# Kernel optimization log

Measured on AMD Instinct MI355X. Metric: run time of the kernel, lower is better.

The kernel has to match this reference:

```python
import jax, jax.numpy as jnp
import numpy as np

V, E, H, B, T = 50257, 1024, 1024, 64, 512  # vocab, embed, hidden, batch, steps
PADDING_TOKEN = 0


def setup_inputs() -> dict:
    key = jax.random.key(0)
    ks = jax.random.split(key, 6)
    s = 0.02
    emb = jax.random.normal(ks[0], (V, E), jnp.float32) * s
    emb = emb.at[PADDING_TOKEN].set(0.0)  # padding_idx row is zero
    W_ih = jax.random.normal(ks[1], (4 * H, E), jnp.float32) * s   # torch LSTMCell weight_ih
    W_hh = jax.random.normal(ks[2], (4 * H, H), jnp.float32) * s   # torch LSTMCell weight_hh
    W_cls = jax.random.normal(ks[3], (V, H), jnp.float32) * s      # classifier weight [out,in]
    b_cls = jnp.zeros((V,), jnp.float32)                            # classifier bias
    batch_reviews = jax.random.randint(ks[4], (B, T), 0, V)
    return dict(batch_reviews=batch_reviews, emb=emb, W_ih=W_ih, W_hh=W_hh,
                W_cls=W_cls, b_cls=b_cls)


def _lstm_scan(x_tbe, W_ih, W_hh):
    # torch.nn.LSTMCell math (bias=False); gate order: i, f, g, o
    Bn = x_tbe.shape[1]
    Hn = W_hh.shape[1]

    def cell(carry, x_be):
        h, c = carry
        gates = x_be @ W_ih.T + h @ W_hh.T              # [B, 4H]
        i, f, g, o = jnp.split(gates, 4, axis=-1)
        c2 = jax.nn.sigmoid(f) * c + jax.nn.sigmoid(i) * jnp.tanh(g)
        h2 = jax.nn.sigmoid(o) * jnp.tanh(c2)
        return (h2, c2), None

    init = (jnp.zeros((Bn, Hn), x_tbe.dtype), jnp.zeros((Bn, Hn), x_tbe.dtype))
    (h, c), _ = jax.lax.scan(cell, init, x_tbe)
    return h, c


def reference(batch_reviews, emb, W_ih, W_hh, W_cls, b_cls):
    x = emb[batch_reviews]               # [B, T, E] embedding lookup
    x_tbe = jnp.transpose(x, (1, 0, 2))  # [T, B, E] for time-major scan
    h, c = _lstm_scan(x_tbe, W_ih, W_hh) # final (h, c) state only
    logits = h @ W_cls.T + b_cls         # [B, V]
    return logits, h, c
```

## Files before the change

kernel.cpp:

```cpp
#include <hip/hip_runtime.h>

#define Bn 64
#define Tn 512
#define En 1024
#define Hn 1024
#define Vn 50257
#define CHUNK 64
#define NCHUNK (Tn / CHUNK)
#define AGENT __HIP_MEMORY_SCOPE_AGENT

typedef __attribute__((ext_vector_type(8))) short short8;
typedef __attribute__((ext_vector_type(4))) float f32x4;
typedef __attribute__((ext_vector_type(4))) unsigned int u32x4;

__device__ __forceinline__ unsigned short f2bf(float f) {
    union { float f; unsigned u; } x; x.f = f;
    unsigned r = x.u + 0x7FFFu + ((x.u >> 16) & 1u);
    return (unsigned short)(r >> 16);
}
__device__ __forceinline__ float bf2f(unsigned short u) {
    union { unsigned u; float f; } x; x.u = ((unsigned)u) << 16; return x.f;
}
__device__ __forceinline__ float sigm(float x) { return 1.0f / (1.0f + __expf(-x)); }
__device__ __forceinline__ float tanh_fast(float x) {
    float e = __expf(2.0f * x);
    return (e - 1.0f) / (e + 1.0f);
}

#define LDH(dst, base, IMM)                                                  \
    asm volatile("global_load_dwordx4 %0, %1, off offset:" #IMM " sc0 sc1"   \
                 : "=v"(dst) : "v"(base) : "memory")
#define VMW(N) do { asm volatile("s_waitcnt vmcnt(" #N ")" ::: "memory");    \
                    __builtin_amdgcn_sched_barrier(0); } while (0)
#define ISSUE_GRP(buf, O0, O1, O2, O3)                                       \
    do {                                                                     \
        LDH((buf)[0], ap0, O0); LDH((buf)[1], ap0, O1);                      \
        LDH((buf)[2], ap0, O2); LDH((buf)[3], ap0, O3);                      \
        LDH((buf)[4], ap1, O0); LDH((buf)[5], ap1, O1);                      \
        LDH((buf)[6], ap1, O2); LDH((buf)[7], ap1, O3);                      \
    } while (0)
#define MFMA_GRP(buf, jb)                                                    \
    do {                                                                     \
        _Pragma("unroll")                                                    \
        for (int jj = 0; jj < 4; ++jj) {                                     \
            union { u32x4 u; short8 s; } f0, f1;                             \
            f0.u = (buf)[jj]; f1.u = (buf)[4 + jj];                          \
            acc[0][0] = __builtin_amdgcn_mfma_f32_16x16x32_bf16(f0.s, breg[0][(jb) + jj], acc[0][0], 0, 0, 0); \
            acc[0][1] = __builtin_amdgcn_mfma_f32_16x16x32_bf16(f0.s, breg[1][(jb) + jj], acc[0][1], 0, 0, 0); \
            acc[1][0] = __builtin_amdgcn_mfma_f32_16x16x32_bf16(f1.s, breg[0][(jb) + jj], acc[1][0], 0, 0, 0); \
            acc[1][1] = __builtin_amdgcn_mfma_f32_16x16x32_bf16(f1.s, breg[1][(jb) + jj], acc[1][1], 0, 0, 0); \
        }                                                                    \
    } while (0)

__global__ __launch_bounds__(256)
void cvt_f32_bf16(const float* __restrict__ src, unsigned short* __restrict__ dst, int n4) {
    int i = blockIdx.x * 256 + threadIdx.x;
    if (i < n4) {
        float4 v = reinterpret_cast<const float4*>(src)[i];
        ushort4 o;
        o.x = f2bf(v.x); o.y = f2bf(v.y); o.z = f2bf(v.z); o.w = f2bf(v.w);
        reinterpret_cast<ushort4*>(dst)[i] = o;
    }
}

__global__ __launch_bounds__(256)
void gather_x(const int* __restrict__ tokens, const float* __restrict__ emb,
              unsigned short* __restrict__ X, int t0) {
    const int r = blockIdx.x;
    const int trel = r >> 6, b = r & 63;
    const int tok = tokens[b * Tn + t0 + trel];
    const float* src = emb + (size_t)tok * En;
    const int k = threadIdx.x * 4;
    float4 v = *reinterpret_cast<const float4*>(src + k);
    ushort4 o;
    o.x = f2bf(v.x); o.y = f2bf(v.y); o.z = f2bf(v.z); o.w = f2bf(v.w);
    *reinterpret_cast<ushort4*>(X + (size_t)r * En + k) = o;
}

__device__ __forceinline__ void gemm_tile(
    const unsigned short* __restrict__ X, const unsigned short* __restrict__ Wih,
    unsigned short* __restrict__ G, int bx, int by,
    unsigned short (*As)[72], unsigned short (*Bs)[72], int tid)
{
    const int w = tid >> 6, l = tid & 63;
    const int wr = w >> 1, wc = w & 1;
    const int koff = (l >> 4) * 8;

    f32x4 acc[4][4];
#pragma unroll
    for (int i = 0; i < 4; ++i)
#pragma unroll
        for (int j = 0; j < 4; ++j) acc[i][j] = (f32x4){0.f, 0.f, 0.f, 0.f};

    for (int kk = 0; kk < En / 64; ++kk) {
        __syncthreads();
#pragma unroll
        for (int j = 0; j < 4; ++j) {
            const int u = tid * 4 + j;
            const int row = u >> 3, ku = (u & 7) * 8;
            *reinterpret_cast<short8*>(&As[row][ku]) =
                *reinterpret_cast<const short8*>(X + (size_t)(by * 128 + row) * En + kk * 64 + ku);
            *reinterpret_cast<short8*>(&Bs[row][ku]) =
                *reinterpret_cast<const short8*>(Wih + (size_t)(bx * 128 + row) * En + kk * 64 + ku);
        }
        __syncthreads();

#pragma unroll
        for (int kc = 0; kc < 2; ++kc) {
            const int k0 = kc * 32 + koff;
            short8 af[4], bf[4];
#pragma unroll
            for (int i = 0; i < 4; ++i)
                af[i] = *reinterpret_cast<const short8*>(&As[wr * 64 + i * 16 + (l & 15)][k0]);
#pragma unroll
            for (int j = 0; j < 4; ++j)
                bf[j] = *reinterpret_cast<const short8*>(&Bs[wc * 64 + j * 16 + (l & 15)][k0]);
#pragma unroll
            for (int i = 0; i < 4; ++i)
#pragma unroll
                for (int j = 0; j < 4; ++j)
                    acc[i][j] = __builtin_amdgcn_mfma_f32_16x16x32_bf16(af[i], bf[j], acc[i][j], 0, 0, 0);
        }
    }

    const int rr = 4 * (l >> 4);
#pragma unroll
    for (int i = 0; i < 4; ++i) {
        const int row = by * 128 + wr * 64 + i * 16 + rr;
#pragma unroll
        for (int j = 0; j < 4; ++j) {
            const int col = bx * 128 + wc * 64 + j * 16 + (l & 15);
#pragma unroll
            for (int r = 0; r < 4; ++r)
                G[(size_t)(row + r) * 4096 + col] = f2bf(acc[i][j][r]);
        }
    }
}

__global__ __launch_bounds__(256)
void gemm_gin(const unsigned short* __restrict__ X, const unsigned short* __restrict__ Wih,
              unsigned short* __restrict__ G) {
    __shared__ __align__(16) unsigned short As[128][72];
    __shared__ __align__(16) unsigned short Bs[128][72];
    gemm_tile(X, Wih, G, blockIdx.x & 31, blockIdx.x >> 5, As, Bs, threadIdx.x);
}

__global__ __launch_bounds__(256, 1)
void lstm_fused(const unsigned short* __restrict__ Gcur, unsigned short* __restrict__ Gnext,
                const unsigned short* __restrict__ Xnext, const unsigned short* __restrict__ Wih,
                const unsigned short* __restrict__ Whh,
                unsigned short* __restrict__ h0, unsigned short* __restrict__ h1,
                float* __restrict__ c_state, unsigned* __restrict__ flags, int t0, int do_gemm,
                float* __restrict__ out_h, float* __restrict__ out_c)
{
    __shared__ __align__(16) char smem[2 * 128 * 72 * 2];

    const int tid = threadIdx.x;

    if (blockIdx.x >= 128) {
        if (!do_gemm) return;
        unsigned short (*As)[72] = reinterpret_cast<unsigned short(*)[72]>(smem);
        unsigned short (*Bs)[72] = reinterpret_cast<unsigned short(*)[72]>(smem + 128 * 72 * 2);
        const int base = (blockIdx.x - 128) * 8;
        for (int tt = 0; tt < 8; ++tt) {
            const int tile = base + tt;
            gemm_tile(Xnext, Wih, Gnext, tile & 31, tile >> 5, As, Bs, tid);
        }
        return;
    }

    typedef float RedT[2][2][64][4];
    RedT* red = reinterpret_cast<RedT*>(smem);

    const int b = blockIdx.x;
    const int w = tid >> 6, l = tid & 63;
    const int kh = w & 1, rh = w >> 1;
    const int koff = (l >> 4) * 8;
    const int lc = l & 15;
    const int hcol = b * 8 + (l & 7);

    short8 breg[2][16];
#pragma unroll
    for (int ct = 0; ct < 2; ++ct) {
        const int gate = ct * 2 + (lc >> 3);
        const unsigned short* wrow = Whh + ((size_t)gate * Hn + (b * 8 + (lc & 7))) * Hn;
#pragma unroll
        for (int j = 0; j < 16; ++j)
            breg[ct][j] = *reinterpret_cast<const short8*>(wrow + (kh * 16 + j) * 32 + koff);
    }

    float c_reg[2][4];
    if (kh == 0) {
#pragma unroll
        for (int rt = 0; rt < 2; ++rt)
#pragma unroll
            for (int r = 0; r < 4; ++r)
                c_reg[rt][r] = c_state[(rh * 32 + rt * 16 + ((l >> 4) << 2) + r) * Hn + hcol];
    }

    const int sg = lc >> 3;
    const int gc0 = sg * Hn + hcol;
    const int gc1 = (2 + sg) * Hn + hcol;

    unsigned short gp0[2][4], gp1[2][4];
    if (kh == 0) {
#pragma unroll
        for (int rt = 0; rt < 2; ++rt) {
            const int rowbase = rh * 32 + rt * 16 + ((l >> 4) << 2);
#pragma unroll
            for (int r = 0; r < 4; ++r) {
                gp0[rt][r] = Gcur[(size_t)(rowbase + r) * 4096 + gc0];
                gp1[rt][r] = Gcur[(size_t)(rowbase + r) * 4096 + gc1];
            }
        }
    }

    for (int s = 0; s < CHUNK; ++s) {
        const int t = t0 + s;
        const unsigned short* hin = (t & 1) ? h1 : h0;
        unsigned short* hout = (t & 1) ? h0 : h1;

        const unsigned short* ap0 =
            hin + (size_t)(rh * 32 + (l & 15)) * Hn + kh * 512 + koff;
        const unsigned short* ap1 =
            hin + (size_t)(rh * 32 + 16 + (l & 15)) * Hn + kh * 512 + koff;

        f32x4 acc[2][2];
        acc[0][0] = acc[0][1] = acc[1][0] = acc[1][1] = (f32x4){0.f, 0.f, 0.f, 0.f};

        u32x4 bufA[8], bufB[8], bufC[8], bufD[8];
        ISSUE_GRP(bufA, 0,   64,  128, 192);
        ISSUE_GRP(bufB, 256, 320, 384, 448);
        ISSUE_GRP(bufC, 512, 576, 640, 704);
        ISSUE_GRP(bufD, 768, 832, 896, 960);

        VMW(24); MFMA_GRP(bufA, 0);
        VMW(16); MFMA_GRP(bufB, 4);
        VMW(8);  MFMA_GRP(bufC, 8);
        VMW(0);  MFMA_GRP(bufD, 12);

        if (kh == 1) {
#pragma unroll
            for (int rt = 0; rt < 2; ++rt)
#pragma unroll
                for (int ct = 0; ct < 2; ++ct)
                    *reinterpret_cast<f32x4*>(&red[rh][rt][ct][l][0]) = acc[rt][ct];
        }
        __syncthreads();

        if (kh == 0) {
#pragma unroll
            for (int rt = 0; rt < 2; ++rt) {
                const int rowbase = rh * 32 + rt * 16 + ((l >> 4) << 2);
                f32x4 a0 = acc[rt][0] + *reinterpret_cast<f32x4*>(&red[rh][rt][0][l][0]);
                f32x4 a1 = acc[rt][1] + *reinterpret_cast<f32x4*>(&red[rh][rt][1][l][0]);
#pragma unroll
                for (int r = 0; r < 4; ++r) {
                    float v0 = a0[r] + bf2f(gp0[rt][r]);
                    float v1 = a1[r] + bf2f(gp1[rt][r]);
                    float p0 = __shfl_xor(v0, 8);
                    float p1 = __shfl_xor(v1, 8);
                    float iv = (l & 8) ? p0 : v0;
                    float fv = (l & 8) ? v0 : p0;
                    float gv = (l & 8) ? p1 : v1;
                    float ov = (l & 8) ? v1 : p1;
                    float cn = sigm(fv) * c_reg[rt][r] + sigm(iv) * tanh_fast(gv);
                    float hn = sigm(ov) * tanh_fast(cn);
                    c_reg[rt][r] = cn;
                    unsigned hb = f2bf(hn);
                    unsigned partner = (unsigned)__shfl_xor((int)hb, 1);
                    if (!(l & 8) && !(l & 1)) {
                        unsigned val = (hb & 0xFFFFu) | (partner << 16);
                        __hip_atomic_store(
                            (unsigned*)(hout + (size_t)(rowbase + r) * Hn + hcol),
                            val, __ATOMIC_RELAXED, AGENT);
                    }
                    if (t == Tn - 1 && !(l & 8)) {
                        out_h[(rowbase + r) * Hn + hcol] = hn;
                        out_c[(rowbase + r) * Hn + hcol] = cn;
                    }
                }
            }
        }

        asm volatile("s_waitcnt vmcnt(0)" ::: "memory");
        __syncthreads();
        if (tid == 0)
            __hip_atomic_store(&flags[b * 32], (unsigned)(t + 1), __ATOMIC_RELAXED, AGENT);

        if (kh == 0 && s + 1 < CHUNK) {
            const unsigned short* Gt = Gcur + (size_t)(s + 1) * Bn * 4096;
#pragma unroll
            for (int rt = 0; rt < 2; ++rt) {
                const int rowbase = rh * 32 + rt * 16 + ((l >> 4) << 2);
#pragma unroll
                for (int r = 0; r < 4; ++r) {
                    gp0[rt][r] = Gt[(size_t)(rowbase + r) * 4096 + gc0];
                    gp1[rt][r] = Gt[(size_t)(rowbase + r) * 4096 + gc1];
                }
            }
        }

        {
            const unsigned target = (unsigned)(t + 1);
            const int pf = (tid & 127) * 32;
            int guard = 0;
            while (__hip_atomic_load(&flags[pf], __ATOMIC_RELAXED, AGENT) < target &&
                   guard < (1 << 16)) {
                __builtin_amdgcn_s_sleep(1);
                ++guard;
            }
        }
        __syncthreads();
    }

    if (kh == 0 && !(l & 8)) {
#pragma unroll
        for (int rt = 0; rt < 2; ++rt)
#pragma unroll
            for (int r = 0; r < 4; ++r)
                c_state[(rh * 32 + rt * 16 + ((l >> 4) << 2) + r) * Hn + hcol] = c_reg[rt][r];
    }
}

__global__ __launch_bounds__(256)
void classifier(const unsigned short* __restrict__ h,
                const float* __restrict__ Wcls, const float* __restrict__ bcls,
                float* __restrict__ logits)
{
    __shared__ __align__(16) unsigned short Al[64][72];
    __shared__ __align__(16) unsigned short Bl[64][72];

    const int tid = threadIdx.x;
    const int v0 = blockIdx.x * 64;
    const int w = tid >> 6, l = tid & 63;
    const int lrow = tid >> 2, q = tid & 3;
    const int v = v0 + lrow;

    const unsigned short* hrow = h + lrow * Hn;
    const float* wrow = Wcls + (size_t)v * Hn;

    f32x4 acc[4];
#pragma unroll
    for (int ct = 0; ct < 4; ++ct) acc[ct] = (f32x4){0.f, 0.f, 0.f, 0.f};

    const int arow = w * 16 + (l & 15);
    const int koff = (l >> 4) * 8;

    for (int ch = 0; ch < 16; ++ch) {
        const int k0 = ch * 64;
        __syncthreads();
#pragma unroll
        for (int i2 = 0; i2 < 4; ++i2) {
            const int k = q * 4 + i2 * 16;
            *reinterpret_cast<ushort4*>(&Al[lrow][k]) =
                *reinterpret_cast<const ushort4*>(hrow + k0 + k);
            if (v < Vn) {
                float4 x = *reinterpret_cast<const float4*>(wrow + k0 + k);
                Bl[lrow][k + 0] = f2bf(x.x); Bl[lrow][k + 1] = f2bf(x.y);
                Bl[lrow][k + 2] = f2bf(x.z); Bl[lrow][k + 3] = f2bf(x.w);
            } else {
                ushort4 z; z.x = z.y = z.z = z.w = 0;
                *reinterpret_cast<ushort4*>(&Bl[lrow][k]) = z;
            }
        }
        __syncthreads();

        short8 a0 = *reinterpret_cast<const short8*>(&Al[arow][koff]);
        short8 a1 = *reinterpret_cast<const short8*>(&Al[arow][32 + koff]);
#pragma unroll
        for (int ct = 0; ct < 4; ++ct) {
            const int bcol = ct * 16 + (l & 15);
            short8 b0 = *reinterpret_cast<const short8*>(&Bl[bcol][koff]);
            short8 b1 = *reinterpret_cast<const short8*>(&Bl[bcol][32 + koff]);
            acc[ct] = __builtin_amdgcn_mfma_f32_16x16x32_bf16(a0, b0, acc[ct], 0, 0, 0);
            acc[ct] = __builtin_amdgcn_mfma_f32_16x16x32_bf16(a1, b1, acc[ct], 0, 0, 0);
        }
    }

    const int rr0 = w * 16 + (l >> 4) * 4;
#pragma unroll
    for (int ct = 0; ct < 4; ++ct) {
        const int vv = v0 + ct * 16 + (l & 15);
        if (vv < Vn) {
            float bb = bcls[vv];
#pragma unroll
            for (int r = 0; r < 4; ++r)
                logits[(size_t)(rr0 + r) * Vn + vv] = acc[ct][r] + bb;
        }
    }
}

extern "C" void kernel_launch(void* const* d_in, const int* in_sizes, int n_in,
                              void* d_out, int out_size, void* d_ws, size_t ws_size,
                              hipStream_t stream)
{
    const int*   tokens = (const int*)d_in[0];
    const float* emb    = (const float*)d_in[1];
    const float* W_ih   = (const float*)d_in[2];
    const float* W_hh   = (const float*)d_in[3];
    const float* W_cls  = (const float*)d_in[4];
    const float* b_cls  = (const float*)d_in[5];
    float* out = (float*)d_out;

    char* ws = (char*)d_ws;
    unsigned short* hbuf0 = (unsigned short*)ws;
    unsigned short* hbuf1 = (unsigned short*)(ws + 131072);
    float*          cst   = (float*)(ws + 262144);
    unsigned*       flags = (unsigned*)(ws + 524288);
    unsigned short* Wih_b = (unsigned short*)(ws + 540672);
    unsigned short* Whh_b = (unsigned short*)(ws + 540672 + 8388608);
    unsigned short* Xb    = (unsigned short*)(ws + 540672 + 2 * 8388608);
    unsigned short* Gb0   = (unsigned short*)(ws + 540672 + 3 * 8388608);
    unsigned short* Gb1   = (unsigned short*)(ws + 540672 + 3 * 8388608 + 33554432);

    hipMemsetAsync(ws, 0, 540672, stream);

    const int n4 = (4 * Hn * En) / 4;
    cvt_f32_bf16<<<n4 / 256, 256, 0, stream>>>(W_ih, Wih_b, n4);
    cvt_f32_bf16<<<n4 / 256, 256, 0, stream>>>(W_hh, Whh_b, n4);

    float* out_h = out + (size_t)Bn * Vn;
    float* out_c = out_h + Bn * Hn;

    gather_x<<<CHUNK * Bn, 256, 0, stream>>>(tokens, emb, Xb, 0);
    gemm_gin<<<32 * 32, 256, 0, stream>>>(Xb, Wih_b, Gb0);

    unsigned short* Gbuf[2] = {Gb0, Gb1};
    for (int c = 0; c < NCHUNK; ++c) {
        const int do_gemm = (c + 1 < NCHUNK) ? 1 : 0;
        if (do_gemm)
            gather_x<<<CHUNK * Bn, 256, 0, stream>>>(tokens, emb, Xb, (c + 1) * CHUNK);
        lstm_fused<<<256, 256, 0, stream>>>(Gbuf[c & 1], Gbuf[(c + 1) & 1], Xb,
                                            Wih_b, Whh_b, hbuf0, hbuf1,
                                            cst, flags, c * CHUNK, do_gemm,
                                            out_h, out_c);
    }

    classifier<<<(Vn + 63) / 64, 256, 0, stream>>>(hbuf0, W_cls, b_cls, out);
}
```

Measured before the change: 4.287 ms.

## Restructure LSTM recurrence to 64 blocks of 512 threads staging h in LDS

The persistent recurrent kernel drops from 128 to 64 recurrent blocks of 512 threads. Each block owns 16 hidden columns across all four gates, with one wave per gate-chunk holding a full K=1024 slice of W_hh in registers. Each step, h is staged through swizzled double-halved LDS buffers instead of per-wave direct global loads. The input-gate GEMM output is re-laid out as time×col×batch so per-step gate prefetches become vectorized 8-byte loads, and GEMM blocks run two tiles concurrently. This aims to cut redundant global h traffic and flag-sync fan-in, but it uses large LDS, higher register pressure from 32 B fragments, and adds extra barriers per step.

New measurement: 4.612 ms. 1.08x slower.

```diff
diff --git a/kernel.cpp b/kernel.cpp
--- a/kernel.cpp
+++ b/kernel.cpp
@@ -27,30 +27,11 @@
     return (e - 1.0f) / (e + 1.0f);
 }
 
-#define LDH(dst, base, IMM)                                                  \
-    asm volatile("global_load_dwordx4 %0, %1, off offset:" #IMM " sc0 sc1"   \
-                 : "=v"(dst) : "v"(base) : "memory")
-#define VMW(N) do { asm volatile("s_waitcnt vmcnt(" #N ")" ::: "memory");    \
-                    __builtin_amdgcn_sched_barrier(0); } while (0)
-#define ISSUE_GRP(buf, O0, O1, O2, O3)                                       \
-    do {                                                                     \
-        LDH((buf)[0], ap0, O0); LDH((buf)[1], ap0, O1);                      \
-        LDH((buf)[2], ap0, O2); LDH((buf)[3], ap0, O3);                      \
-        LDH((buf)[4], ap1, O0); LDH((buf)[5], ap1, O1);                      \
-        LDH((buf)[6], ap1, O2); LDH((buf)[7], ap1, O3);                      \
-    } while (0)
-#define MFMA_GRP(buf, jb)                                                    \
-    do {                                                                     \
-        _Pragma("unroll")                                                    \
-        for (int jj = 0; jj < 4; ++jj) {                                     \
-            union { u32x4 u; short8 s; } f0, f1;                             \
-            f0.u = (buf)[jj]; f1.u = (buf)[4 + jj];                          \
-            acc[0][0] = __builtin_amdgcn_mfma_f32_16x16x32_bf16(f0.s, breg[0][(jb) + jj], acc[0][0], 0, 0, 0); \
-            acc[0][1] = __builtin_amdgcn_mfma_f32_16x16x32_bf16(f0.s, breg[1][(jb) + jj], acc[0][1], 0, 0, 0); \
-            acc[1][0] = __builtin_amdgcn_mfma_f32_16x16x32_bf16(f1.s, breg[0][(jb) + jj], acc[1][0], 0, 0, 0); \
-            acc[1][1] = __builtin_amdgcn_mfma_f32_16x16x32_bf16(f1.s, breg[1][(jb) + jj], acc[1][1], 0, 0, 0); \
-        }                                                                    \
-    } while (0)
+#define LDHA(dst, addr)                                                      \
+    asm volatile("global_load_dwordx4 %0, %1, off sc0 sc1"                   \
+                 : "=v"(dst) : "v"(addr) : "memory")
+#define VMW0 do { asm volatile("s_waitcnt vmcnt(0)" ::: "memory");           \
+                  __builtin_amdgcn_sched_barrier(0); } while (0)
 
 __global__ __launch_bounds__(256)
 void cvt_f32_bf16(const float* __restrict__ src, unsigned short* __restrict__ dst, int n4) {
@@ -79,7 +60,7 @@
 
 __device__ __forceinline__ void gemm_tile(
     const unsigned short* __restrict__ X, const unsigned short* __restrict__ Wih,
-    unsigned short* __restrict__ G, int bx, int by,
+    unsigned short* __restrict__ G2, int bx, int by,
     unsigned short (*As)[72], unsigned short (*Bs)[72], int tid)
 {
     const int w = tid >> 6, l = tid & 63;
@@ -126,26 +107,28 @@
     const int rr = 4 * (l >> 4);
 #pragma unroll
     for (int i = 0; i < 4; ++i) {
-        const int row = by * 128 + wr * 64 + i * 16 + rr;
+        const int grow = by * 128 + wr * 64 + i * 16 + rr;
+        const int sI = grow >> 6, br = grow & 63;
 #pragma unroll
         for (int j = 0; j < 4; ++j) {
             const int col = bx * 128 + wc * 64 + j * 16 + (l & 15);
-#pragma unroll
-            for (int r = 0; r < 4; ++r)
-                G[(size_t)(row + r) * 4096 + col] = f2bf(acc[i][j][r]);
+            ushort4 o;
+            o.x = f2bf(acc[i][j][0]); o.y = f2bf(acc[i][j][1]);
+            o.z = f2bf(acc[i][j][2]); o.w = f2bf(acc[i][j][3]);
+            *reinterpret_cast<ushort4*>(G2 + (size_t)sI * 262144 + (size_t)col * 64 + br) = o;
         }
     }
 }
 
 __global__ __launch_bounds__(256)
 void gemm_gin(const unsigned short* __restrict__ X, const unsigned short* __restrict__ Wih,
-              unsigned short* __restrict__ G) {
+              unsigned short* __restrict__ G2) {
     __shared__ __align__(16) unsigned short As[128][72];
     __shared__ __align__(16) unsigned short Bs[128][72];
-    gemm_tile(X, Wih, G, blockIdx.x & 31, blockIdx.x >> 5, As, Bs, threadIdx.x);
-}
-
-__global__ __launch_bounds__(256, 1)
+    gemm_tile(X, Wih, G2, blockIdx.x & 31, blockIdx.x >> 5, As, Bs, threadIdx.x);
+}
+
+__global__ __launch_bounds__(512, 1)
 void lstm_fused(const unsigned short* __restrict__ Gcur, unsigned short* __restrict__ Gnext,
                 const unsigned short* __restrict__ Xnext, const unsigned short* __restrict__ Wih,
                 const unsigned short* __restrict__ Whh,
@@ -153,129 +136,158 @@
                 float* __restrict__ c_state, unsigned* __restrict__ flags, int t0, int do_gemm,
                 float* __restrict__ out_h, float* __restrict__ out_c)
 {
-    __shared__ __align__(16) char smem[2 * 128 * 72 * 2];
+    __shared__ __align__(16) char smem[143360];
 
     const int tid = threadIdx.x;
 
-    if (blockIdx.x >= 128) {
+    if (blockIdx.x >= 64) {
         if (!do_gemm) return;
-        unsigned short (*As)[72] = reinterpret_cast<unsigned short(*)[72]>(smem);
-        unsigned short (*Bs)[72] = reinterpret_cast<unsigned short(*)[72]>(smem + 128 * 72 * 2);
-        const int base = (blockIdx.x - 128) * 8;
-        for (int tt = 0; tt < 8; ++tt) {
-            const int tile = base + tt;
-            gemm_tile(Xnext, Wih, Gnext, tile & 31, tile >> 5, As, Bs, tid);
+        const int sub = tid >> 8, stid = tid & 255;
+        unsigned short (*As)[72] = reinterpret_cast<unsigned short(*)[72]>(smem + sub * 36864);
+        unsigned short (*Bs)[72] = reinterpret_cast<unsigned short(*)[72]>(smem + sub * 36864 + 18432);
+        const int base = (blockIdx.x - 64) * 8;
+        for (int it = 0; it < 4; ++it) {
+            const int tile = base + it * 2 + sub;
+            gemm_tile(Xnext, Wih, Gnext, tile & 31, tile >> 5, As, Bs, stid);
         }
         return;
     }
 
-    typedef float RedT[2][2][64][4];
-    RedT* red = reinterpret_cast<RedT*>(smem);
+    char* const hS0 = smem;
+    char* const hS1 = smem + 65536;
+    float* const red = reinterpret_cast<float*>(smem + 131072);
 
     const int b = blockIdx.x;
     const int w = tid >> 6, l = tid & 63;
-    const int kh = w & 1, rh = w >> 1;
+    const int rh = w >> 2, ch = w & 3;
     const int koff = (l >> 4) * 8;
-    const int lc = l & 15;
-    const int hcol = b * 8 + (l & 7);
-
-    short8 breg[2][16];
-#pragma unroll
-    for (int ct = 0; ct < 2; ++ct) {
-        const int gate = ct * 2 + (lc >> 3);
-        const unsigned short* wrow = Whh + ((size_t)gate * Hn + (b * 8 + (lc & 7))) * Hn;
-#pragma unroll
-        for (int j = 0; j < 16; ++j)
-            breg[ct][j] = *reinterpret_cast<const short8*>(wrow + (kh * 16 + j) * 32 + koff);
+    const int hcol = b * 16 + (l & 15);
+    const int gcol = ch * Hn + hcol;
+
+    short8 breg[32];
+    {
+        const unsigned short* wr_ = Whh + ((size_t)(ch * Hn) + hcol) * Hn + koff;
+#pragma unroll
+        for (int j = 0; j < 32; ++j)
+            breg[j] = *reinterpret_cast<const short8*>(wr_ + j * 32);
     }
 
     float c_reg[2][4];
-    if (kh == 0) {
-#pragma unroll
-        for (int rt = 0; rt < 2; ++rt)
-#pragma unroll
-            for (int r = 0; r < 4; ++r)
-                c_reg[rt][r] = c_state[(rh * 32 + rt * 16 + ((l >> 4) << 2) + r) * Hn + hcol];
-    }
-
-    const int sg = lc >> 3;
-    const int gc0 = sg * Hn + hcol;
-    const int gc1 = (2 + sg) * Hn + hcol;
-
-    unsigned short gp0[2][4], gp1[2][4];
-    if (kh == 0) {
+    if (ch == 0) {
 #pragma unroll
         for (int rt = 0; rt < 2; ++rt) {
             const int rowbase = rh * 32 + rt * 16 + ((l >> 4) << 2);
 #pragma unroll
-            for (int r = 0; r < 4; ++r) {
-                gp0[rt][r] = Gcur[(size_t)(rowbase + r) * 4096 + gc0];
-                gp1[rt][r] = Gcur[(size_t)(rowbase + r) * 4096 + gc1];
-            }
-        }
+            for (int r = 0; r < 4; ++r)
+                c_reg[rt][r] = c_state[(rowbase + r) * Hn + hcol];
+        }
+    }
+
+    ushort4 gp[2];
+#pragma unroll
+    for (int rt = 0; rt < 2; ++rt) {
+        const int rowbase = rh * 32 + rt * 16 + ((l >> 4) << 2);
+        gp[rt] = *reinterpret_cast<const ushort4*>(Gcur + (size_t)gcol * 64 + rowbase);
     }
 
     for (int s = 0; s < CHUNK; ++s) {
         const int t = t0 + s;
         const unsigned short* hin = (t & 1) ? h1 : h0;
         unsigned short* hout = (t & 1) ? h0 : h1;
-
-        const unsigned short* ap0 =
-            hin + (size_t)(rh * 32 + (l & 15)) * Hn + kh * 512 + koff;
-        const unsigned short* ap1 =
-            hin + (size_t)(rh * 32 + 16 + (l & 15)) * Hn + kh * 512 + koff;
-
-        f32x4 acc[2][2];
-        acc[0][0] = acc[0][1] = acc[1][0] = acc[1][1] = (f32x4){0.f, 0.f, 0.f, 0.f};
-
-        u32x4 bufA[8], bufB[8], bufC[8], bufD[8];
-        ISSUE_GRP(bufA, 0,   64,  128, 192);
-        ISSUE_GRP(bufB, 256, 320, 384, 448);
-        ISSUE_GRP(bufC, 512, 576, 640, 704);
-        ISSUE_GRP(bufD, 768, 832, 896, 960);
-
-        VMW(24); MFMA_GRP(bufA, 0);
-        VMW(16); MFMA_GRP(bufB, 4);
-        VMW(8);  MFMA_GRP(bufC, 8);
-        VMW(0);  MFMA_GRP(bufD, 12);
-
-        if (kh == 1) {
-#pragma unroll
-            for (int rt = 0; rt < 2; ++rt)
-#pragma unroll
-                for (int ct = 0; ct < 2; ++ct)
-                    *reinterpret_cast<f32x4*>(&red[rh][rt][ct][l][0]) = acc[rt][ct];
-        }
-        __syncthreads();
-
-        if (kh == 0) {
+        const char* hinB = (const char*)hin;
+
+        f32x4 acc[2];
+        acc[0] = (f32x4){0.f, 0.f, 0.f, 0.f};
+        acc[1] = (f32x4){0.f, 0.f, 0.f, 0.f};
+
+        u32x4 sb[8];
+#pragma unroll
+        for (int i = 0; i < 8; ++i) {
+            const int u = tid + i * 512;
+            LDHA(sb[i], hinB + (u >> 6) * 2048 + ((u & 63) * 16));
+        }
+        VMW0;
+#pragma unroll
+        for (int i = 0; i < 8; ++i) {
+            const int u = tid + i * 512;
+            const int row = u >> 6, kb = (u & 63) * 16;
+            *reinterpret_cast<u32x4*>(hS0 + ((row * 1024 + kb) ^ ((row & 15) << 4))) = sb[i];
+        }
+        __syncthreads();
+
+#pragma unroll
+        for (int i = 0; i < 8; ++i) {
+            const int u = tid + i * 512;
+            LDHA(sb[i], hinB + (u >> 6) * 2048 + 1024 + ((u & 63) * 16));
+        }
+
+#pragma unroll
+        for (int jj = 0; jj < 16; ++jj) {
+#pragma unroll
+            for (int rt = 0; rt < 2; ++rt) {
+                const int row = rh * 32 + rt * 16 + (l & 15);
+                const int kb = jj * 64 + (l >> 4) * 16;
+                short8 af = *reinterpret_cast<const short8*>(
+                    hS0 + ((row * 1024 + kb) ^ ((row & 15) << 4)));
+                acc[rt] = __builtin_amdgcn_mfma_f32_16x16x32_bf16(af, breg[jj], acc[rt], 0, 0, 0);
+            }
+        }
+
+        VMW0;
+#pragma unroll
+        for (int i = 0; i < 8; ++i) {
+            const int u = tid + i * 512;
+            const int row = u >> 6, kb = (u & 63) * 16;
+            *reinterpret_cast<u32x4*>(hS1 + ((row * 1024 + kb) ^ ((row & 15) << 4))) = sb[i];
+        }
+        __syncthreads();
+
+#pragma unroll
+        for (int jj = 0; jj < 16; ++jj) {
+#pragma unroll
+            for (int rt = 0; rt < 2; ++rt) {
+                const int row = rh * 32 + rt * 16 + (l & 15);
+                const int kb = jj * 64 + (l >> 4) * 16;
+                short8 af = *reinterpret_cast<const short8*>(
+                    hS1 + ((row * 1024 + kb) ^ ((row & 15) << 4)));
+                acc[rt] = __builtin_amdgcn_mfma_f32_16x16x32_bf16(af, breg[16 + jj], acc[rt], 0, 0, 0);
+            }
+        }
+
+        if (ch != 0) {
+#pragma unroll
+            for (int rt = 0; rt < 2; ++rt) {
+                f32x4 v = acc[rt];
+                v[0] += bf2f(gp[rt].x); v[1] += bf2f(gp[rt].y);
+                v[2] += bf2f(gp[rt].z); v[3] += bf2f(gp[rt].w);
+                *reinterpret_cast<f32x4*>(red + (((rh * 3 + (ch - 1)) * 2 + rt) * 64 + l) * 4) = v;
+            }
+        }
+        __syncthreads();
+
+        if (ch == 0) {
 #pragma unroll
             for (int rt = 0; rt < 2; ++rt) {
                 const int rowbase = rh * 32 + rt * 16 + ((l >> 4) << 2);
-                f32x4 a0 = acc[rt][0] + *reinterpret_cast<f32x4*>(&red[rh][rt][0][l][0]);
-                f32x4 a1 = acc[rt][1] + *reinterpret_cast<f32x4*>(&red[rh][rt][1][l][0]);
+                f32x4 fv4 = *reinterpret_cast<f32x4*>(red + (((rh * 3 + 0) * 2 + rt) * 64 + l) * 4);
+                f32x4 gv4 = *reinterpret_cast<f32x4*>(red + (((rh * 3 + 1) * 2 + rt) * 64 + l) * 4);
+                f32x4 ov4 = *reinterpret_cast<f32x4*>(red + (((rh * 3 + 2) * 2 + rt) * 64 + l) * 4);
+                const unsigned short gpi[4] = {gp[rt].x, gp[rt].y, gp[rt].z, gp[rt].w};
 #pragma unroll
                 for (int r = 0; r < 4; ++r) {
-                    float v0 = a0[r] + bf2f(gp0[rt][r]);
-                    float v1 = a1[r] + bf2f(gp1[rt][r]);
-                    float p0 = __shfl_xor(v0, 8);
-                    float p1 = __shfl_xor(v1, 8);
-                    float iv = (l & 8) ? p0 : v0;
-                    float fv = (l & 8) ? v0 : p0;
-                    float gv = (l & 8) ? p1 : v1;
-                    float ov = (l & 8) ? v1 : p1;
-                    float cn = sigm(fv) * c_reg[rt][r] + sigm(iv) * tanh_fast(gv);
-                    float hn = sigm(ov) * tanh_fast(cn);
+                    float iv = acc[rt][r] + bf2f(gpi[r]);
+                    float cn = sigm(fv4[r]) * c_reg[rt][r] + sigm(iv) * tanh_fast(gv4[r]);
+                    float hn = sigm(ov4[r]) * tanh_fast(cn);
                     c_reg[rt][r] = cn;
                     unsigned hb = f2bf(hn);
                     unsigned partner = (unsigned)__shfl_xor((int)hb, 1);
-                    if (!(l & 8) && !(l & 1)) {
+                    if (!(l & 1)) {
                         unsigned val = (hb & 0xFFFFu) | (partner << 16);
                         __hip_atomic_store(
                             (unsigned*)(hout + (size_t)(rowbase + r) * Hn + hcol),
                             val, __ATOMIC_RELAXED, AGENT);
                     }
-                    if (t == Tn - 1 && !(l & 8)) {
+                    if (t == Tn - 1) {
                         out_h[(rowbase + r) * Hn + hcol] = hn;
                         out_c[(rowbase + r) * Hn + hcol] = cn;
                     }
@@ -287,23 +299,17 @@
         __syncthreads();
         if (tid == 0)
             __hip_atomic_store(&flags[b * 32], (unsigned)(t + 1), __ATOMIC_RELAXED, AGENT);
-
-        if (kh == 0 && s + 1 < CHUNK) {
-            const unsigned short* Gt = Gcur + (size_t)(s + 1) * Bn * 4096;
+        if (s + 1 < CHUNK) {
+            const unsigned short* G1 = Gcur + (size_t)(s + 1) * 262144;
 #pragma unroll
             for (int rt = 0; rt < 2; ++rt) {
                 const int rowbase = rh * 32 + rt * 16 + ((l >> 4) << 2);
-#pragma unroll
-                for (int r = 0; r < 4; ++r) {
-                    gp0[rt][r] = Gt[(size_t)(rowbase + r) * 4096 + gc0];
-                    gp1[rt][r] = Gt[(size_t)(rowbase + r) * 4096 + gc1];
-                }
-            }
-        }
-
+                gp[rt] = *reinterpret_cast<const ushort4*>(G1 + (size_t)gcol * 64 + rowbase);
+            }
+        }
         {
             const unsigned target = (unsigned)(t + 1);
-            const int pf = (tid & 127) * 32;
+            const int pf = (tid & 63) * 32;
             int guard = 0;
             while (__hip_atomic_load(&flags[pf], __ATOMIC_RELAXED, AGENT) < target &&
                    guard < (1 << 16)) {
@@ -314,12 +320,14 @@
         __syncthreads();
     }
 
-    if (kh == 0 && !(l & 8)) {
-#pragma unroll
-        for (int rt = 0; rt < 2; ++rt)
+    if (ch == 0) {
+#pragma unroll
+        for (int rt = 0; rt < 2; ++rt) {
+            const int rowbase = rh * 32 + rt * 16 + ((l >> 4) << 2);
 #pragma unroll
             for (int r = 0; r < 4; ++r)
-                c_state[(rh * 32 + rt * 16 + ((l >> 4) << 2) + r) * Hn + hcol] = c_reg[rt][r];
+                c_state[(rowbase + r) * Hn + hcol] = c_reg[rt][r];
+        }
     }
 }
 
@@ -431,7 +439,7 @@
         const int do_gemm = (c + 1 < NCHUNK) ? 1 : 0;
         if (do_gemm)
             gather_x<<<CHUNK * Bn, 256, 0, stream>>>(tokens, emb, Xb, (c + 1) * CHUNK);
-        lstm_fused<<<256, 256, 0, stream>>>(Gbuf[c & 1], Gbuf[(c + 1) & 1], Xb,
+        lstm_fused<<<192, 512, 0, stream>>>(Gbuf[c & 1], Gbuf[(c + 1) & 1], Xb,
                                             Wih_b, Whh_b, hbuf0, hbuf1,
                                             cst, flags, c * CHUNK, do_gemm,
                                             out_h, out_c);
```

## Split batch into two halves with separate flags to overlap recurrent steps

Applied to the files above, without the earlier changes.

The persistent LSTM step is split into two batch halves (rows 0-31 and 32-63), each with its own readiness flag array and its own reduction buffer. A block now waits only for the half it is about to load, then computes, publishes and signals half A before finishing half B. Work on half A of one step can therefore overlap with other blocks still producing half B, which shortens the grid-wide barrier on the critical path. In exchange there are two syncthreads and flag waits per step instead of one, and MFMA batching per wave drops from four accumulators to two.

After: 4.116 ms. 1.04x faster.

```diff
diff --git a/kernel.cpp b/kernel.cpp
--- a/kernel.cpp
+++ b/kernel.cpp
@@ -32,24 +32,38 @@
                  : "=v"(dst) : "v"(base) : "memory")
 #define VMW(N) do { asm volatile("s_waitcnt vmcnt(" #N ")" ::: "memory");    \
                     __builtin_amdgcn_sched_barrier(0); } while (0)
-#define ISSUE_GRP(buf, O0, O1, O2, O3)                                       \
+#define ISSUE16(buf, ap)                                                     \
     do {                                                                     \
-        LDH((buf)[0], ap0, O0); LDH((buf)[1], ap0, O1);                      \
-        LDH((buf)[2], ap0, O2); LDH((buf)[3], ap0, O3);                      \
-        LDH((buf)[4], ap1, O0); LDH((buf)[5], ap1, O1);                      \
-        LDH((buf)[6], ap1, O2); LDH((buf)[7], ap1, O3);                      \
+        LDH((buf)[0],  ap, 0);   LDH((buf)[1],  ap, 64);                     \
+        LDH((buf)[2],  ap, 128); LDH((buf)[3],  ap, 192);                    \
+        LDH((buf)[4],  ap, 256); LDH((buf)[5],  ap, 320);                    \
+        LDH((buf)[6],  ap, 384); LDH((buf)[7],  ap, 448);                    \
+        LDH((buf)[8],  ap, 512); LDH((buf)[9],  ap, 576);                    \
+        LDH((buf)[10], ap, 640); LDH((buf)[11], ap, 704);                    \
+        LDH((buf)[12], ap, 768); LDH((buf)[13], ap, 832);                    \
+        LDH((buf)[14], ap, 896); LDH((buf)[15], ap, 960);                    \
     } while (0)
-#define MFMA_GRP(buf, jb)                                                    \
+#define MFMA16(buf, a0, a1)                                                  \
     do {                                                                     \
         _Pragma("unroll")                                                    \
-        for (int jj = 0; jj < 4; ++jj) {                                     \
-            union { u32x4 u; short8 s; } f0, f1;                             \
-            f0.u = (buf)[jj]; f1.u = (buf)[4 + jj];                          \
-            acc[0][0] = __builtin_amdgcn_mfma_f32_16x16x32_bf16(f0.s, breg[0][(jb) + jj], acc[0][0], 0, 0, 0); \
-            acc[0][1] = __builtin_amdgcn_mfma_f32_16x16x32_bf16(f0.s, breg[1][(jb) + jj], acc[0][1], 0, 0, 0); \
-            acc[1][0] = __builtin_amdgcn_mfma_f32_16x16x32_bf16(f1.s, breg[0][(jb) + jj], acc[1][0], 0, 0, 0); \
-            acc[1][1] = __builtin_amdgcn_mfma_f32_16x16x32_bf16(f1.s, breg[1][(jb) + jj], acc[1][1], 0, 0, 0); \
+        for (int jj = 0; jj < 16; ++jj) {                                    \
+            union { u32x4 u; short8 s; } fz; fz.u = (buf)[jj];               \
+            a0 = __builtin_amdgcn_mfma_f32_16x16x32_bf16(fz.s, breg[0][jj], a0, 0, 0, 0); \
+            a1 = __builtin_amdgcn_mfma_f32_16x16x32_bf16(fz.s, breg[1][jj], a1, 0, 0, 0); \
         }                                                                    \
+    } while (0)
+#define POLL128(F, tgt)                                                      \
+    do {                                                                     \
+        unsigned fa_ = __hip_atomic_load(&(F)[l * 32], __ATOMIC_RELAXED, AGENT);       \
+        unsigned fb_ = __hip_atomic_load(&(F)[(64 + l) * 32], __ATOMIC_RELAXED, AGENT);\
+        int g_ = 0;                                                          \
+        while (__any((fa_ < (unsigned)(tgt)) || (fb_ < (unsigned)(tgt))) && g_ < (1 << 16)) { \
+            __builtin_amdgcn_s_sleep(1);                                     \
+            fa_ = __hip_atomic_load(&(F)[l * 32], __ATOMIC_RELAXED, AGENT);            \
+            fb_ = __hip_atomic_load(&(F)[(64 + l) * 32], __ATOMIC_RELAXED, AGENT);     \
+            ++g_;                                                            \
+        }                                                                    \
+        __builtin_amdgcn_sched_barrier(0);                                   \
     } while (0)
 
 __global__ __launch_bounds__(256)
@@ -150,7 +164,8 @@
                 const unsigned short* __restrict__ Xnext, const unsigned short* __restrict__ Wih,
                 const unsigned short* __restrict__ Whh,
                 unsigned short* __restrict__ h0, unsigned short* __restrict__ h1,
-                float* __restrict__ c_state, unsigned* __restrict__ flags, int t0, int do_gemm,
+                float* __restrict__ c_state, unsigned* __restrict__ flagsA,
+                unsigned* __restrict__ flagsB, int t0, int do_gemm,
                 float* __restrict__ out_h, float* __restrict__ out_c)
 {
     __shared__ __align__(16) char smem[2 * 128 * 72 * 2];
@@ -170,7 +185,8 @@
     }
 
     typedef float RedT[2][2][64][4];
-    RedT* red = reinterpret_cast<RedT*>(smem);
+    RedT* redA = reinterpret_cast<RedT*>(smem);
+    RedT* redB = reinterpret_cast<RedT*>(smem + 4096);
 
     const int b = blockIdx.x;
     const int w = tid >> 6, l = tid & 63;
@@ -189,137 +205,151 @@
             breg[ct][j] = *reinterpret_cast<const short8*>(wrow + (kh * 16 + j) * 32 + koff);
     }
 
-    float c_reg[2][4];
+    const int rowbase = rh * 16 + ((l >> 4) << 2);
+
+    float cA[4], cB[4];
     if (kh == 0) {
 #pragma unroll
-        for (int rt = 0; rt < 2; ++rt)
-#pragma unroll
-            for (int r = 0; r < 4; ++r)
-                c_reg[rt][r] = c_state[(rh * 32 + rt * 16 + ((l >> 4) << 2) + r) * Hn + hcol];
+        for (int r = 0; r < 4; ++r) {
+            cA[r] = c_state[(rowbase + r) * Hn + hcol];
+            cB[r] = c_state[(32 + rowbase + r) * Hn + hcol];
+        }
     }
 
     const int sg = lc >> 3;
     const int gc0 = sg * Hn + hcol;
     const int gc1 = (2 + sg) * Hn + hcol;
 
-    unsigned short gp0[2][4], gp1[2][4];
+    unsigned short gA0[4], gA1[4], gB0[4], gB1[4];
     if (kh == 0) {
 #pragma unroll
-        for (int rt = 0; rt < 2; ++rt) {
-            const int rowbase = rh * 32 + rt * 16 + ((l >> 4) << 2);
-#pragma unroll
-            for (int r = 0; r < 4; ++r) {
-                gp0[rt][r] = Gcur[(size_t)(rowbase + r) * 4096 + gc0];
-                gp1[rt][r] = Gcur[(size_t)(rowbase + r) * 4096 + gc1];
-            }
-        }
-    }
+        for (int r = 0; r < 4; ++r) {
+            gA0[r] = Gcur[(size_t)(rowbase + r) * 4096 + gc0];
+            gA1[r] = Gcur[(size_t)(rowbase + r) * 4096 + gc1];
+            gB0[r] = Gcur[(size_t)(32 + rowbase + r) * 4096 + gc0];
+            gB1[r] = Gcur[(size_t)(32 + rowbase + r) * 4096 + gc1];
+        }
+    }
+
+    const int arow = rh * 16 + (l & 15);
 
     for (int s = 0; s < CHUNK; ++s) {
         const int t = t0 + s;
         const unsigned short* hin = (t & 1) ? h1 : h0;
         unsigned short* hout = (t & 1) ? h0 : h1;
 
-        const unsigned short* ap0 =
-            hin + (size_t)(rh * 32 + (l & 15)) * Hn + kh * 512 + koff;
-        const unsigned short* ap1 =
-            hin + (size_t)(rh * 32 + 16 + (l & 15)) * Hn + kh * 512 + koff;
-
-        f32x4 acc[2][2];
-        acc[0][0] = acc[0][1] = acc[1][0] = acc[1][1] = (f32x4){0.f, 0.f, 0.f, 0.f};
-
-        u32x4 bufA[8], bufB[8], bufC[8], bufD[8];
-        ISSUE_GRP(bufA, 0,   64,  128, 192);
-        ISSUE_GRP(bufB, 256, 320, 384, 448);
-        ISSUE_GRP(bufC, 512, 576, 640, 704);
-        ISSUE_GRP(bufD, 768, 832, 896, 960);
-
-        VMW(24); MFMA_GRP(bufA, 0);
-        VMW(16); MFMA_GRP(bufB, 4);
-        VMW(8);  MFMA_GRP(bufC, 8);
-        VMW(0);  MFMA_GRP(bufD, 12);
-
+        POLL128(flagsA, t);
+        const unsigned short* apA = hin + (size_t)arow * Hn + kh * 512 + koff;
+        u32x4 bufA[16];
+        ISSUE16(bufA, apA);
+
+        POLL128(flagsB, t);
+        const unsigned short* apB = hin + (size_t)(32 + arow) * Hn + kh * 512 + koff;
+        u32x4 bufB[16];
+        ISSUE16(bufB, apB);
+
+        f32x4 aA0 = (f32x4){0.f, 0.f, 0.f, 0.f};
+        f32x4 aA1 = (f32x4){0.f, 0.f, 0.f, 0.f};
+        MFMA16(bufA, aA0, aA1);
         if (kh == 1) {
-#pragma unroll
-            for (int rt = 0; rt < 2; ++rt)
-#pragma unroll
-                for (int ct = 0; ct < 2; ++ct)
-                    *reinterpret_cast<f32x4*>(&red[rh][rt][ct][l][0]) = acc[rt][ct];
-        }
-        __syncthreads();
-
+            *reinterpret_cast<f32x4*>(&(*redA)[rh][0][l][0]) = aA0;
+            *reinterpret_cast<f32x4*>(&(*redA)[rh][1][l][0]) = aA1;
+        }
+        __syncthreads();
         if (kh == 0) {
-#pragma unroll
-            for (int rt = 0; rt < 2; ++rt) {
-                const int rowbase = rh * 32 + rt * 16 + ((l >> 4) << 2);
-                f32x4 a0 = acc[rt][0] + *reinterpret_cast<f32x4*>(&red[rh][rt][0][l][0]);
-                f32x4 a1 = acc[rt][1] + *reinterpret_cast<f32x4*>(&red[rh][rt][1][l][0]);
-#pragma unroll
-                for (int r = 0; r < 4; ++r) {
-                    float v0 = a0[r] + bf2f(gp0[rt][r]);
-                    float v1 = a1[r] + bf2f(gp1[rt][r]);
-                    float p0 = __shfl_xor(v0, 8);
-                    float p1 = __shfl_xor(v1, 8);
-                    float iv = (l & 8) ? p0 : v0;
-                    float fv = (l & 8) ? v0 : p0;
-                    float gv = (l & 8) ? p1 : v1;
-                    float ov = (l & 8) ? v1 : p1;
-                    float cn = sigm(fv) * c_reg[rt][r] + sigm(iv) * tanh_fast(gv);
-                    float hn = sigm(ov) * tanh_fast(cn);
-                    c_reg[rt][r] = cn;
-                    unsigned hb = f2bf(hn);
-                    unsigned partner = (unsigned)__shfl_xor((int)hb, 1);
-                    if (!(l & 8) && !(l & 1)) {
-                        unsigned val = (hb & 0xFFFFu) | (partner << 16);
-                        __hip_atomic_store(
-                            (unsigned*)(hout + (size_t)(rowbase + r) * Hn + hcol),
-                            val, __ATOMIC_RELAXED, AGENT);
-                    }
-                    if (t == Tn - 1 && !(l & 8)) {
-                        out_h[(rowbase + r) * Hn + hcol] = hn;
-                        out_c[(rowbase + r) * Hn + hcol] = cn;
-                    }
+            f32x4 a0 = aA0 + *reinterpret_cast<f32x4*>(&(*redA)[rh][0][l][0]);
+            f32x4 a1 = aA1 + *reinterpret_cast<f32x4*>(&(*redA)[rh][1][l][0]);
+#pragma unroll
+            for (int r = 0; r < 4; ++r) {
+                float v0 = a0[r] + bf2f(gA0[r]);
+                float v1 = a1[r] + bf2f(gA1[r]);
+                float p0 = __shfl_xor(v0, 8);
+                float p1 = __shfl_xor(v1, 8);
+                float iv = (l & 8) ? p0 : v0;
+                float fv = (l & 8) ? v0 : p0;
+                float gv = (l & 8) ? p1 : v1;
+                float ov = (l & 8) ? v1 : p1;
+                float cn = sigm(fv) * cA[r] + sigm(iv) * tanh_fast(gv);
+                float hn = sigm(ov) * tanh_fast(cn);
+                cA[r] = cn;
+                unsigned hb = f2bf(hn);
+                unsigned partner = (unsigned)__shfl_xor((int)hb, 1);
+                if (!(l & 8) && !(l & 1)) {
+                    unsigned val = (hb & 0xFFFFu) | (partner << 16);
+                    __hip_atomic_store((unsigned*)(hout + (size_t)(rowbase + r) * Hn + hcol),
+                                       val, __ATOMIC_RELAXED, AGENT);
+                }
+                if (t == Tn - 1 && !(l & 8)) {
+                    out_h[(rowbase + r) * Hn + hcol] = hn;
+                    out_c[(rowbase + r) * Hn + hcol] = cn;
                 }
             }
         }
-
         asm volatile("s_waitcnt vmcnt(0)" ::: "memory");
         __syncthreads();
         if (tid == 0)
-            __hip_atomic_store(&flags[b * 32], (unsigned)(t + 1), __ATOMIC_RELAXED, AGENT);
+            __hip_atomic_store(&flagsA[b * 32], (unsigned)(t + 1), __ATOMIC_RELAXED, AGENT);
+
+        f32x4 aB0 = (f32x4){0.f, 0.f, 0.f, 0.f};
+        f32x4 aB1 = (f32x4){0.f, 0.f, 0.f, 0.f};
+        MFMA16(bufB, aB0, aB1);
+        if (kh == 1) {
+            *reinterpret_cast<f32x4*>(&(*redB)[rh][0][l][0]) = aB0;
+            *reinterpret_cast<f32x4*>(&(*redB)[rh][1][l][0]) = aB1;
+        }
+        __syncthreads();
+        if (kh == 0) {
+            f32x4 a0 = aB0 + *reinterpret_cast<f32x4*>(&(*redB)[rh][0][l][0]);
+            f32x4 a1 = aB1 + *reinterpret_cast<f32x4*>(&(*redB)[rh][1][l][0]);
+#pragma unroll
+            for (int r = 0; r < 4; ++r) {
+                float v0 = a0[r] + bf2f(gB0[r]);
+                float v1 = a1[r] + bf2f(gB1[r]);
+                float p0 = __shfl_xor(v0, 8);
+                float p1 = __shfl_xor(v1, 8);
+                float iv = (l & 8) ? p0 : v0;
+                float fv = (l & 8) ? v0 : p0;
+                float gv = (l & 8) ? p1 : v1;
+                float ov = (l & 8) ? v1 : p1;
+                float cn = sigm(fv) * cB[r] + sigm(iv) * tanh_fast(gv);
+                float hn = sigm(ov) * tanh_fast(cn);
+                cB[r] = cn;
+                unsigned hb = f2bf(hn);
+                unsigned partner = (unsigned)__shfl_xor((int)hb, 1);
+                if (!(l & 8) && !(l & 1)) {
+                    unsigned val = (hb & 0xFFFFu) | (partner << 16);
+                    __hip_atomic_store((unsigned*)(hout + (size_t)(32 + rowbase + r) * Hn + hcol),
+                                       val, __ATOMIC_RELAXED, AGENT);
+                }
+                if (t == Tn - 1 && !(l & 8)) {
+                    out_h[(32 + rowbase + r) * Hn + hcol] = hn;
+                    out_c[(32 + rowbase + r) * Hn + hcol] = cn;
+                }
+            }
+        }
+        asm volatile("s_waitcnt vmcnt(0)" ::: "memory");
+        __syncthreads();
+        if (tid == 0)
+            __hip_atomic_store(&flagsB[b * 32], (unsigned)(t + 1), __ATOMIC_RELAXED, AGENT);
 
         if (kh == 0 && s + 1 < CHUNK) {
             const unsigned short* Gt = Gcur + (size_t)(s + 1) * Bn * 4096;
 #pragma unroll
-            for (int rt = 0; rt < 2; ++rt) {
-                const int rowbase = rh * 32 + rt * 16 + ((l >> 4) << 2);
-#pragma unroll
-                for (int r = 0; r < 4; ++r) {
-                    gp0[rt][r] = Gt[(size_t)(rowbase + r) * 4096 + gc0];
-                    gp1[rt][r] = Gt[(size_t)(rowbase + r) * 4096 + gc1];
-                }
+            for (int r = 0; r < 4; ++r) {
+                gA0[r] = Gt[(size_t)(rowbase + r) * 4096 + gc0];
+                gA1[r] = Gt[(size_t)(rowbase + r) * 4096 + gc1];
+                gB0[r] = Gt[(size_t)(32 + rowbase + r) * 4096 + gc0];
+                gB1[r] = Gt[(size_t)(32 + rowbase + r) * 4096 + gc1];
             }
         }
-
-        {
-            const unsigned target = (unsigned)(t + 1);
-            const int pf = (tid & 127) * 32;
-            int guard = 0;
-            while (__hip_atomic_load(&flags[pf], __ATOMIC_RELAXED, AGENT) < target &&
-                   guard < (1 << 16)) {
-                __builtin_amdgcn_s_sleep(1);
-                ++guard;
-            }
-        }
-        __syncthreads();
     }
 
     if (kh == 0 && !(l & 8)) {
 #pragma unroll
-        for (int rt = 0; rt < 2; ++rt)
-#pragma unroll
-            for (int r = 0; r < 4; ++r)
-                c_state[(rh * 32 + rt * 16 + ((l >> 4) << 2) + r) * Hn + hcol] = c_reg[rt][r];
+        for (int r = 0; r < 4; ++r) {
+            c_state[(rowbase + r) * Hn + hcol] = cA[r];
+            c_state[(32 + rowbase + r) * Hn + hcol] = cB[r];
+        }
     }
 }
 
@@ -404,17 +434,18 @@
     float* out = (float*)d_out;
 
     char* ws = (char*)d_ws;
-    unsigned short* hbuf0 = (unsigned short*)ws;
-    unsigned short* hbuf1 = (unsigned short*)(ws + 131072);
-    float*          cst   = (float*)(ws + 262144);
-    unsigned*       flags = (unsigned*)(ws + 524288);
-    unsigned short* Wih_b = (unsigned short*)(ws + 540672);
-    unsigned short* Whh_b = (unsigned short*)(ws + 540672 + 8388608);
-    unsigned short* Xb    = (unsigned short*)(ws + 540672 + 2 * 8388608);
-    unsigned short* Gb0   = (unsigned short*)(ws + 540672 + 3 * 8388608);
-    unsigned short* Gb1   = (unsigned short*)(ws + 540672 + 3 * 8388608 + 33554432);
-
-    hipMemsetAsync(ws, 0, 540672, stream);
+    unsigned short* hbuf0  = (unsigned short*)ws;
+    unsigned short* hbuf1  = (unsigned short*)(ws + 131072);
+    float*          cst    = (float*)(ws + 262144);
+    unsigned*       flagsA = (unsigned*)(ws + 524288);
+    unsigned*       flagsB = (unsigned*)(ws + 540672);
+    unsigned short* Wih_b  = (unsigned short*)(ws + 557056);
+    unsigned short* Whh_b  = (unsigned short*)(ws + 557056 + 8388608);
+    unsigned short* Xb     = (unsigned short*)(ws + 557056 + 2 * 8388608);
+    unsigned short* Gb0    = (unsigned short*)(ws + 557056 + 3 * 8388608);
+    unsigned short* Gb1    = (unsigned short*)(ws + 557056 + 3 * 8388608 + 33554432);
+
+    hipMemsetAsync(ws, 0, 557056, stream);
 
     const int n4 = (4 * Hn * En) / 4;
     cvt_f32_bf16<<<n4 / 256, 256, 0, stream>>>(W_ih, Wih_b, n4);
@@ -433,7 +464,7 @@
             gather_x<<<CHUNK * Bn, 256, 0, stream>>>(tokens, emb, Xb, (c + 1) * CHUNK);
         lstm_fused<<<256, 256, 0, stream>>>(Gbuf[c & 1], Gbuf[(c + 1) & 1], Xb,
                                             Wih_b, Whh_b, hbuf0, hbuf1,
-                                            cst, flags, c * CHUNK, do_gemm,
+                                            cst, flagsA, flagsB, c * CHUNK, do_gemm,
                                             out_h, out_c);
     }
 
```
